# Optimization experiments

Measured on AMD Instinct MI355X. Metric: run time of the kernel, lower is better.

The kernel has to match this reference:

```python
import jax, jax.numpy as jnp
import numpy as np
from jax import lax

WIN_SIZE = 11
SIGMA = 1.5
WEIGHTS = jnp.array([0.0448, 0.2856, 0.3001, 0.2363, 0.1333], dtype=jnp.float32)
C1 = (0.01 * 1.0) ** 2  # val_range = 1.0
C2 = (0.03 * 1.0) ** 2


def gaussian_kernel2d(kernel_size, sigma):
    g = jnp.arange(kernel_size, dtype=jnp.float32) - kernel_size // 2
    g = jnp.exp(-(g ** 2) / (2.0 * sigma ** 2))
    g = g / g.sum()
    return jnp.outer(g, g)  # [k, k]


def depthwise_conv(x, k2d):
    # x: [B, C, H, W]; same gaussian window applied per-channel (groups=C), VALID padding
    C = x.shape[1]
    w = jnp.broadcast_to(k2d, (C, 1) + k2d.shape).astype(x.dtype)
    return lax.conv_general_dilated(x, w, (1, 1), 'VALID',
                                    feature_group_count=C,
                                    dimension_numbers=('NCHW', 'OIHW', 'NCHW'))


def ssim_index(x, y, k2d, nonnegative=True):
    # returns (ss, cs) each of shape [B, C] (spatial mean, per channel)
    m1 = depthwise_conv(x, k2d)
    m2 = depthwise_conv(y, k2d)
    m12 = m1 * m2
    m1s = m1 * m1
    m2s = m2 * m2
    v1 = depthwise_conv(x * x, k2d) - m1s
    v2 = depthwise_conv(y * y, k2d) - m2s
    cov = depthwise_conv(x * y, k2d) - m12
    cs = (2.0 * cov + C2) / (v1 + v2 + C2)
    ss = (2.0 * m12 + C1) / (m1s + m2s + C1) * cs
    ss = ss.reshape(ss.shape[0], ss.shape[1], -1).mean(axis=-1)
    cs = cs.reshape(cs.shape[0], cs.shape[1], -1).mean(axis=-1)
    if nonnegative:
        ss = jnp.maximum(ss, 0.0)
        cs = jnp.maximum(cs, 0.0)
    return ss, cs


def avg_pool2(x):
    # F.avg_pool2d(kernel_size=2). Input spatial dims are even at every scale
    # (512 -> 32), so ceil_mode never pads; plain 2x2/2 mean pooling is exact.
    s = lax.reduce_window(x, jnp.array(0.0, x.dtype), lax.add,
                          (1, 1, 2, 2), (1, 1, 2, 2), 'VALID')
    return s * 0.25


def setup_inputs() -> dict:
    key = jax.random.key(0)
    k1, k2 = jax.random.split(key)
    B, C, H, W = 4, 12, 512, 512
    pred = jax.random.normal(k1, (B, C, H, W), dtype=jnp.float32)
    target = jax.random.randint(k2, (B, H, W), 0, C, dtype=jnp.int64)
    return {"pred": pred, "target": target}


def reference(pred, target):
    # MS_SSIMLoss.forward with process_input=True, nonnegative=True.
    # The per-class python loop in the original is an independent depthwise
    # computation per channel -> vectorized here as a C-channel grouped conv;
    # loss = mean over classes of (1 - mean over batch of msss) == 1 - mean(msss).
    num_classes = pred.shape[1]
    x = jax.nn.softmax(pred, axis=1)
    y = jax.nn.one_hot(target, num_classes, dtype=pred.dtype).transpose(0, 3, 1, 2)
    k2d = gaussian_kernel2d(WIN_SIZE, SIGMA)
    m = WEIGHTS.shape[0]
    vals = []
    for i in range(m):
        if i > 0:
            x = avg_pool2(x)
            y = avg_pool2(y)
        ss, cs = ssim_index(x, y, k2d, nonnegative=True)
        vals.append(cs if i + 1 < m else ss)
    stacked = jnp.stack(vals, axis=-1)  # [B, C, m]
    msss = jnp.prod(stacked ** WEIGHTS, axis=-1)  # [B, C]
    return 1.0 - msss.mean()
```

## Files before the change

kernel.cpp:

```cpp
#include <hip/hip_runtime.h>

#define NCH 12
#define NB  4
#define BC  48
#define HW0 (512 * 512)

#define GK_INIT { 0.00102840f, 0.00759863f, 0.03600078f, 0.10936081f, \
                  0.21300541f, 0.26601164f, 0.21300541f, 0.10936081f, \
                  0.03600078f, 0.00759863f, 0.00102840f }

__global__ __launch_bounds__(256)
void k_prep(const float* __restrict__ pred, const int* __restrict__ tgt,
            float* __restrict__ U, float* __restrict__ X1,
            unsigned short* __restrict__ Y1, double* __restrict__ acc) {
    if (blockIdx.x == 0) {
        for (int t = threadIdx.x; t < 480; t += 256) acc[t] = 0.0;
    }
    const int blk = blockIdx.x;
    const int b  = blk >> 8;
    const int py = blk & 255;
    const int px = threadIdx.x;
    const size_t o00 = (size_t)(2 * py) * 512 + 2 * px;
    const size_t o10 = o00 + 512;
    const float* Pb = pred + (size_t)b * NCH * HW0;

    float s00 = 0.f, s01 = 0.f, s10 = 0.f, s11 = 0.f;
#pragma unroll
    for (int c = 0; c < NCH; ++c) {
        const float* pc = Pb + (size_t)c * HW0;
        float2 r0 = *(const float2*)(pc + o00);
        float2 r1 = *(const float2*)(pc + o10);
        s00 += __expf(r0.x); s01 += __expf(r0.y);
        s10 += __expf(r1.x); s11 += __expf(r1.y);
    }
    float u00 = 1.f / s00, u01 = 1.f / s01, u10 = 1.f / s10, u11 = 1.f / s11;
    float* Ub = U + (size_t)b * HW0;
    *(float2*)(Ub + o00) = make_float2(u00, u01);
    *(float2*)(Ub + o10) = make_float2(u10, u11);

    const int* Tb = tgt + (size_t)b * HW0;
    int2 t0 = *(const int2*)(Tb + o00);
    int2 t1 = *(const int2*)(Tb + o10);

#pragma unroll
    for (int c = 0; c < NCH; ++c) {
        const float* pc = Pb + (size_t)c * HW0;
        float2 r0 = *(const float2*)(pc + o00);
        float2 r1 = *(const float2*)(pc + o10);
        float xs = __expf(r0.x) * u00 + __expf(r0.y) * u01
                 + __expf(r1.x) * u10 + __expf(r1.y) * u11;
        size_t oidx = ((size_t)(b * NCH + c) * 256 + py) * 256 + px;
        X1[oidx] = 0.25f * xs;
        unsigned cnt = (unsigned)(t0.x == c) + (unsigned)(t0.y == c)
                     + (unsigned)(t1.x == c) + (unsigned)(t1.y == c);
        Y1[oidx] = (unsigned short)(cnt << 6);
    }
}

union SMem {
    struct {
        float sx[42 * 43 + 4];
        uint2 tm4[42 * 35];
        unsigned long long ybits[30];
        float red[8];
    } s0;
    struct {
        float sx[42 * 43 + 4];
        uint2 tm4[42 * 35];
        unsigned short tm5[42 * 35];
        unsigned short syu[42 * 43 + 4];
        float red[8];
    } rg;
};

__device__ __forceinline__ void ssim0_tile(
    const float* __restrict__ pred, const float* __restrict__ U,
    const int* __restrict__ tgt, double* __restrict__ acc,
    int tile, int bc,
    float* sx, uint2* tm4, unsigned long long* ybits, float* red) {
    constexpr int SS = 43;
    constexpr int TS = 35;
    constexpr int H = 512, W = 512, OH = 502, OW = 502, tilesX = 16;
    const float gk[11] = GK_INIT;

    const int ty = tile / tilesX, tx = tile - ty * tilesX;
    const int oy = ty * 32, ox = tx * 32;
    const int tid = threadIdx.x;
    const bool interior = (oy + 41 < H) && (ox + 41 < W);

    const int b = bc / NCH, cls = bc - (bc / NCH) * NCH;
    const float* Pb = pred + (((size_t)b * NCH + cls) << 18);
    const float* Ub = U + ((size_t)b << 18);
    const int* Tb = tgt + ((size_t)b << 18);

    {
        int r = tid / 42, c = tid - (tid / 42) * 42;
#pragma unroll
        for (int k = 0; k < 7; ++k) {
            bool inr = (k < 6) || (tid < 228);
            int gy = oy + r, gx = ox + c;
            bool ld = inr && (interior || (gy < H && gx < W));
            float xv = 0.f;
            bool bit = false;
            if (ld) {
                int off = gy * W + gx;
                xv = expf(Pb[off]) * Ub[off];
                bit = (Tb[off] == cls);
            }
            unsigned long long mk = __ballot(bit);
            if ((tid & 63) == 0) ybits[(tid >> 6) + (k << 2)] = mk;
            if (inr) sx[r * SS + c] = xv;
            c += 4; r += 6;
            if (c >= 42) { c -= 42; r += 1; }
        }
        if (tid == 0) { ybits[28] = 0ull; ybits[29] = 0ull; }
    }
    __syncthreads();

    if (tid < 252) {
        int rr = tid / 6, s = tid - (tid / 6) * 6;
        int c0 = s * 6;
        const float* px = sx + rr * SS + c0;
        float ac0[6] = {}, ac1[6] = {}, ac2[6] = {}, ac3[6] = {};
        unsigned long long win;
        {
            int i0 = rr * 42 + c0;
            int w = i0 >> 6, sh = i0 & 63;
            unsigned long long lo = ybits[w], hi = ybits[w + 1];
            win = sh ? ((lo >> sh) | (hi << (64 - sh))) : lo;
        }
#pragma unroll
        for (int j = 0; j < 16; ++j) {
            float xv = px[j];
            float xx = xv * xv;
            bool bit = (win >> j) & 1;
            float yv = bit ? 1.f : 0.f;
            float xy = bit ? xv : 0.f;
#pragma unroll
            for (int o = 0; o < 6; ++o) {
                int kk = j - o;
                if (kk >= 0 && kk <= 10) {
                    float g = gk[kk];
                    ac0[o] = fmaf(g, xv, ac0[o]);
                    ac1[o] = fmaf(g, yv, ac1[o]);
                    ac2[o] = fmaf(g, xx, ac2[o]);
                    ac3[o] = fmaf(g, xy, ac3[o]);
                }
            }
        }
        int ob = rr * TS + c0;
#pragma unroll
        for (int o = 0; o < 6; ++o) {
            if (c0 + o < 32) {
                unsigned ua = __float_as_uint(ac0[o]);
                unsigned ub = __float_as_uint(ac1[o]);
                unsigned uc = __float_as_uint(ac2[o]);
                unsigned ud = __float_as_uint(ac3[o]);
                tm4[ob + o] = make_uint2((ua >> 16) | (ub & 0xFFFF0000u),
                                         (uc >> 16) | (ud & 0xFFFF0000u));
            }
        }
    }
    __syncthreads();

    const float C1 = 1e-4f, C2 = 9e-4f;
    const int cc = tid & 31, rg = tid >> 5, r0 = rg << 2;
    float a0[4] = {}, a1[4] = {}, a2[4] = {}, a3[4] = {};
    const int vb = r0 * TS + cc;
#pragma unroll
    for (int k = 0; k < 14; ++k) {
        uint2 tv = tm4[vb + k * TS];
        float m1v = __uint_as_float(tv.x << 16);
        float m2v = __uint_as_float(tv.x & 0xFFFF0000u);
        float xxv = __uint_as_float(tv.y << 16);
        float xyv = __uint_as_float(tv.y & 0xFFFF0000u);
#pragma unroll
        for (int j = 0; j < 4; ++j) {
            int kk = k - j;
            if (kk >= 0 && kk <= 10) {
                float g = gk[kk];
                a0[j] = fmaf(g, m1v, a0[j]);
                a1[j] = fmaf(g, m2v, a1[j]);
                a2[j] = fmaf(g, xxv, a2[j]);
                a3[j] = fmaf(g, xyv, a3[j]);
            }
        }
    }
    float cs_l = 0.f, ss_l = 0.f;
    const bool colok = (ox + cc < OW);
#pragma unroll
    for (int j = 0; j < 4; ++j) {
        if (colok && (oy + r0 + j < OH)) {
            float m1 = a0[j], m2 = a1[j];
            float sxx = a2[j], sxy_ = a3[j];
            float m11 = m1 * m1, m22 = m2 * m2, m12 = m1 * m2;
            float v1 = sxx - m11, v2 = m2 - m22, cov = sxy_ - m12;
            float d1 = m11 + m22 + C1, d2 = v1 + v2 + C2;
            float n2 = 2.f * cov + C2;
            float q = 1.f / (d1 * d2);
            cs_l = fmaf(n2 * d1, q, cs_l);
            ss_l = fmaf((2.f * m12 + C1) * n2, q, ss_l);
        }
    }

    for (int off = 32; off; off >>= 1) {
        cs_l += __shfl_down(cs_l, off);
        ss_l += __shfl_down(ss_l, off);
    }
    int wv = tid >> 6, ln = tid & 63;
    if (ln == 0) { red[wv] = cs_l; red[4 + wv] = ss_l; }
    __syncthreads();
    if (tid == 0) {
        double cs_b = (double)red[0] + (double)red[1] + (double)red[2] + (double)red[3];
        double ss_b = (double)red[4] + (double)red[5] + (double)red[6] + (double)red[7];
        atomicAdd(&acc[bc], cs_b);
        atomicAdd(&acc[48 + bc], ss_b);
    }
}

template <int PIN>
__device__ __forceinline__ void ssim_tile_g(
    const float* __restrict__ Xs, const unsigned short* __restrict__ Ys,
    int H, int W, int OH, int OW, int tilesX, int tile, int bc,
    double* __restrict__ acc, int scale,
    float* sx, uint2* tm4, unsigned short* tm5, unsigned short* syu, float* red) {
    constexpr int SS = 43;
    constexpr int TS = 35;
    const float gk[11] = GK_INIT;

    const int ty = tile / tilesX, tx = tile - ty * tilesX;
    const int oy = ty * 32, ox = tx * 32;
    const int tid = threadIdx.x;
    const bool interior = (oy + 41 < H) && (ox + 41 < W);

    constexpr int SC = 1 << PIN;
    const int SW = W * SC;
    const float* Xb = Xs + (size_t)bc * H * W * SC * SC;
    const unsigned short* Yb = Ys + (size_t)bc * H * W * SC * SC;

    {
        int r = tid / 42, c = tid - (tid / 42) * 42;
#pragma unroll
        for (int k = 0; k < 7; ++k) {
            bool inr = (k < 6) || (tid < 228);
            int gy = oy + r, gx = ox + c;
            bool ld = inr && (interior || (gy < H && gx < W));
            float xv = 0.f;
            unsigned short yv = 0;
            if (ld) {
                if constexpr (PIN == 0) {
                    int off = gy * SW + gx;
                    xv = Xb[off];
                    yv = Yb[off];
                } else {
                    const float* q = Xb + (SC * gy) * SW + SC * gx;
                    const unsigned short* qy = Yb + (SC * gy) * SW + SC * gx;
                    float s = 0.f; unsigned us = 0;
#pragma unroll
                    for (int a = 0; a < SC; ++a) {
                        const float* qr = q + a * SW;
                        const unsigned short* qyr = qy + a * SW;
                        if constexpr (PIN == 1) {
                            float2 f = *(const float2*)qr;
                            s += f.x + f.y;
                            ushort2 uy = *(const ushort2*)qyr;
                            us += (unsigned)uy.x + (unsigned)uy.y;
                        } else {
#pragma unroll
                            for (int e4 = 0; e4 < SC / 4; ++e4) {
                                float4 f = *(const float4*)(qr + e4 * 4);
                                s += (f.x + f.y) + (f.z + f.w);
                                ushort4 uy = *(const ushort4*)(qyr + e4 * 4);
                                us += ((unsigned)uy.x + (unsigned)uy.y)
                                    + ((unsigned)uy.z + (unsigned)uy.w);
                            }
                        }
                    }
                    xv = s * (1.f / (float)(SC * SC));
                    yv = (unsigned short)(us >> (2 * PIN));
                }
            }
            if (inr) { sx[r * SS + c] = xv; syu[r * SS + c] = yv; }
            c += 4; r += 6;
            if (c >= 42) { c -= 42; r += 1; }
        }
    }
    __syncthreads();

    if (tid < 252) {
        int rr = tid / 6, s = tid - (tid / 6) * 6;
        int c0 = s * 6;
        const float* px = sx + rr * SS + c0;
        const unsigned short* pyu = syu + rr * SS + c0;
        float ac0[6] = {}, ac1[6] = {}, ac2[6] = {}, ac3[6] = {}, ac4[6] = {};
#pragma unroll
        for (int j = 0; j < 16; ++j) {
            float xv = px[j];
            float xx = xv * xv;
            float yv = (float)pyu[j];
            float xy = xv * yv;
            float yy = yv * yv;
#pragma unroll
            for (int o = 0; o < 6; ++o) {
                int kk = j - o;
                if (kk >= 0 && kk <= 10) {
                    float g = gk[kk];
                    ac0[o] = fmaf(g, xv, ac0[o]);
                    ac1[o] = fmaf(g, yv, ac1[o]);
                    ac2[o] = fmaf(g, xx, ac2[o]);
                    ac3[o] = fmaf(g, xy, ac3[o]);
                    ac4[o] = fmaf(g, yy, ac4[o]);
                }
            }
        }
        int ob = rr * TS + c0;
#pragma unroll
        for (int o = 0; o < 6; ++o) {
            if (c0 + o < 32) {
                unsigned ua = __float_as_uint(ac0[o]) + 0x8000u;
                unsigned ub = __float_as_uint(ac1[o]) + 0x8000u;
                unsigned uc = __float_as_uint(ac2[o]) + 0x8000u;
                unsigned ud = __float_as_uint(ac3[o]) + 0x8000u;
                unsigned ue = __float_as_uint(ac4[o]) + 0x8000u;
                tm4[ob + o] = make_uint2((ua >> 16) | (ub & 0xFFFF0000u),
                                         (uc >> 16) | (ud & 0xFFFF0000u));
                tm5[ob + o] = (unsigned short)(ue >> 16);
            }
        }
    }
    __syncthreads();

    const float C1 = 1e-4f, C2 = 9e-4f;
    const int cc = tid & 31, rg = tid >> 5, r0 = rg << 2;
    float a0[4] = {}, a1[4] = {}, a2[4] = {}, a3[4] = {}, a4[4] = {};
    const int vb = r0 * TS + cc;
#pragma unroll
    for (int k = 0; k < 14; ++k) {
        uint2 tv = tm4[vb + k * TS];
        float t0 = __uint_as_float(tv.x << 16);
        float t1 = __uint_as_float(tv.x & 0xFFFF0000u);
        float t2 = __uint_as_float(tv.y << 16);
        float t3 = __uint_as_float(tv.y & 0xFFFF0000u);
        float t4 = __uint_as_float((unsigned)tm5[vb + k * TS] << 16);
#pragma unroll
        for (int j = 0; j < 4; ++j) {
            int kk = k - j;
            if (kk >= 0 && kk <= 10) {
                float g = gk[kk];
                a0[j] = fmaf(g, t0, a0[j]);
                a1[j] = fmaf(g, t1, a1[j]);
                a2[j] = fmaf(g, t2, a2[j]);
                a3[j] = fmaf(g, t3, a3[j]);
                a4[j] = fmaf(g, t4, a4[j]);
            }
        }
    }
    float cs_l = 0.f, ss_l = 0.f;
    const bool colok = (ox + cc < OW);
#pragma unroll
    for (int j = 0; j < 4; ++j) {
        if (colok && (oy + r0 + j < OH)) {
            float m1 = a0[j];
            float m2 = a1[j] * (1.f / 256.f);
            float sxx = a2[j];
            float sxy_ = a3[j] * (1.f / 256.f);
            float syy_ = a4[j] * (1.f / 65536.f);
            float m11 = m1 * m1, m22 = m2 * m2, m12 = m1 * m2;
            float v1 = sxx - m11, v2 = syy_ - m22, cov = sxy_ - m12;
            float d1 = m11 + m22 + C1, d2 = v1 + v2 + C2;
            float n2 = 2.f * cov + C2;
            float q = 1.f / (d1 * d2);
            cs_l = fmaf(n2 * d1, q, cs_l);
            ss_l = fmaf((2.f * m12 + C1) * n2, q, ss_l);
        }
    }

    for (int offs = 32; offs; offs >>= 1) {
        cs_l += __shfl_down(cs_l, offs);
        ss_l += __shfl_down(ss_l, offs);
    }
    int wv = tid >> 6, ln = tid & 63;
    if (ln == 0) { red[wv] = cs_l; red[4 + wv] = ss_l; }
    __syncthreads();
    if (tid == 0) {
        double cs_b = (double)red[0] + (double)red[1] + (double)red[2] + (double)red[3];
        double ss_b = (double)red[4] + (double)red[5] + (double)red[6] + (double)red[7];
        atomicAdd(&acc[scale * 96 + bc], cs_b);
        atomicAdd(&acc[scale * 96 + 48 + bc], ss_b);
    }
}

__global__ __launch_bounds__(256, 6)
void k_main(const float* __restrict__ pred, const float* __restrict__ U,
            const int* __restrict__ tgt,
            const float* __restrict__ X1, const unsigned short* __restrict__ Y1,
            double* __restrict__ acc) {
    __shared__ SMem sm;
    const int gb = blockIdx.x;

    int s0_idx = -1, rest_idx = -1;
    if (gb < 16320) {
        int r = gb & 3, q = gb >> 2;
        if (r == 0) rest_idx = q;
        else        s0_idx = 3 * q + (r - 1);
    } else {
        s0_idx = 12240 + (gb - 16320);
    }

    if (s0_idx >= 0) {
        ssim0_tile(pred, U, tgt, acc, s0_idx & 255, s0_idx >> 8,
                   sm.s0.sx, sm.s0.tm4, sm.s0.ybits, sm.s0.red);
        return;
    }
    const int gq = rest_idx;
    if (gq < 48) {
        ssim_tile_g<3>(X1, Y1, 32, 32, 22, 22, 1, 0, gq,
                       acc, 4, sm.rg.sx, sm.rg.tm4, sm.rg.tm5, sm.rg.syu, sm.rg.red);
    } else if (gq < 240) {
        int t = gq - 48;
        ssim_tile_g<2>(X1, Y1, 64, 64, 54, 54, 2, t & 3, t >> 2,
                       acc, 3, sm.rg.sx, sm.rg.tm4, sm.rg.tm5, sm.rg.syu, sm.rg.red);
    } else if (gq < 1008) {
        int t = gq - 240;
        ssim_tile_g<1>(X1, Y1, 128, 128, 118, 118, 4, t & 15, t >> 4,
                       acc, 2, sm.rg.sx, sm.rg.tm4, sm.rg.tm5, sm.rg.syu, sm.rg.red);
    } else {
        int t = gq - 1008;
        ssim_tile_g<0>(X1, Y1, 256, 256, 246, 246, 8, t & 63, t >> 6,
                       acc, 1, sm.rg.sx, sm.rg.tm4, sm.rg.tm5, sm.rg.syu, sm.rg.red);
    }
}

__global__ void k_final(const double* __restrict__ acc, float* __restrict__ out) {
    const float wts[5] = {0.0448f, 0.2856f, 0.3001f, 0.2363f, 0.1333f};
    const float cnt[5] = {252004.f, 60516.f, 13924.f, 2916.f, 484.f};
    int tid = threadIdx.x;
    float msss = 0.f;
    if (tid < BC) {
        msss = 1.f;
#pragma unroll
        for (int s = 0; s < 5; ++s) {
            double a = (s < 4) ? acc[s * 96 + tid] : acc[s * 96 + 48 + tid];
            float v = fmaxf((float)(a / (double)cnt[s]), 0.f);
            msss *= powf(v, wts[s]);
        }
    }
    for (int off = 32; off; off >>= 1) msss += __shfl_down(msss, off);
    if (tid == 0) out[0] = 1.f - msss * (1.f / (float)BC);
}

extern "C" void kernel_launch(void* const* d_in, const int* in_sizes, int n_in,
                              void* d_out, int out_size, void* d_ws, size_t ws_size,
                              hipStream_t stream) {
    const float* pred = (const float*)d_in[0];
    const int*   tgt  = (const int*)d_in[1];
    float* out = (float*)d_out;

    double* acc = (double*)d_ws;
    float* U  = (float*)(acc + 480);
    float* X1 = U + (size_t)NB * HW0;
    unsigned short* Y1 = (unsigned short*)(X1 + (size_t)BC * 65536);

    k_prep<<<1024, 256, 0, stream>>>(pred, tgt, U, X1, Y1, acc);

    k_main<<<16368, 256, 0, stream>>>(pred, U, tgt, X1, Y1, acc);

    k_final<<<1, 64, 0, stream>>>(acc, out);
}
```

Before: 235.4 us.

## Cache softmax exps, pack x/y into one LDS word, fast exp, raise occupancy

k_prep now keeps the 12 per-channel exponentials in registers instead of reloading pred and recomputing exp in a second pass. In the coarse-scale tiles, x is rounded to bf16 and packed with the y count into a single 32-bit LDS word, which shrinks shared memory and halves LDS reads in the conv loop. Scale 0 switches expf to __expf, and launch bounds go from 6 to 7 blocks per CU. The bf16 rounding of x and the fast exp lower accuracy, and the tighter register cap could cause spills.

```diff
diff --git a/kernel.cpp b/kernel.cpp
--- a/kernel.cpp
+++ b/kernel.cpp
@@ -24,14 +24,16 @@
     const size_t o10 = o00 + 512;
     const float* Pb = pred + (size_t)b * NCH * HW0;
 
+    float ex[NCH], ey[NCH], ez[NCH], ew[NCH];
     float s00 = 0.f, s01 = 0.f, s10 = 0.f, s11 = 0.f;
 #pragma unroll
     for (int c = 0; c < NCH; ++c) {
         const float* pc = Pb + (size_t)c * HW0;
         float2 r0 = *(const float2*)(pc + o00);
         float2 r1 = *(const float2*)(pc + o10);
-        s00 += __expf(r0.x); s01 += __expf(r0.y);
-        s10 += __expf(r1.x); s11 += __expf(r1.y);
+        ex[c] = __expf(r0.x); ey[c] = __expf(r0.y);
+        ez[c] = __expf(r1.x); ew[c] = __expf(r1.y);
+        s00 += ex[c]; s01 += ey[c]; s10 += ez[c]; s11 += ew[c];
     }
     float u00 = 1.f / s00, u01 = 1.f / s01, u10 = 1.f / s10, u11 = 1.f / s11;
     float* Ub = U + (size_t)b * HW0;
@@ -44,11 +46,7 @@
 
 #pragma unroll
     for (int c = 0; c < NCH; ++c) {
-        const float* pc = Pb + (size_t)c * HW0;
-        float2 r0 = *(const float2*)(pc + o00);
-        float2 r1 = *(const float2*)(pc + o10);
-        float xs = __expf(r0.x) * u00 + __expf(r0.y) * u01
-                 + __expf(r1.x) * u10 + __expf(r1.y) * u11;
+        float xs = ex[c] * u00 + ey[c] * u01 + ez[c] * u10 + ew[c] * u11;
         size_t oidx = ((size_t)(b * NCH + c) * 256 + py) * 256 + px;
         X1[oidx] = 0.25f * xs;
         unsigned cnt = (unsigned)(t0.x == c) + (unsigned)(t0.y == c)
@@ -65,10 +63,9 @@
         float red[8];
     } s0;
     struct {
-        float sx[42 * 43 + 4];
+        unsigned int sxy[42 * 43 + 4];
         uint2 tm4[42 * 35];
         unsigned short tm5[42 * 35];
-        unsigned short syu[42 * 43 + 4];
         float red[8];
     } rg;
 };
@@ -104,7 +101,7 @@
             bool bit = false;
             if (ld) {
                 int off = gy * W + gx;
-                xv = expf(Pb[off]) * Ub[off];
+                xv = __expf(Pb[off]) * Ub[off];
                 bit = (Tb[off] == cls);
             }
             unsigned long long mk = __ballot(bit);
@@ -223,7 +220,7 @@
     const float* __restrict__ Xs, const unsigned short* __restrict__ Ys,
     int H, int W, int OH, int OW, int tilesX, int tile, int bc,
     double* __restrict__ acc, int scale,
-    float* sx, uint2* tm4, unsigned short* tm5, unsigned short* syu, float* red) {
+    unsigned int* sxy, uint2* tm4, unsigned short* tm5, float* red) {
     constexpr int SS = 43;
     constexpr int TS = 35;
     const float gk[11] = GK_INIT;
@@ -246,12 +243,12 @@
             int gy = oy + r, gx = ox + c;
             bool ld = inr && (interior || (gy < H && gx < W));
             float xv = 0.f;
-            unsigned short yv = 0;
+            unsigned yc = 0;
             if (ld) {
                 if constexpr (PIN == 0) {
                     int off = gy * SW + gx;
                     xv = Xb[off];
-                    yv = Yb[off];
+                    yc = Yb[off];
                 } else {
                     const float* q = Xb + (SC * gy) * SW + SC * gx;
                     const unsigned short* qy = Yb + (SC * gy) * SW + SC * gx;
@@ -277,10 +274,13 @@
                         }
                     }
                     xv = s * (1.f / (float)(SC * SC));
-                    yv = (unsigned short)(us >> (2 * PIN));
+                    yc = us >> (2 * PIN);
                 }
             }
-            if (inr) { sx[r * SS + c] = xv; syu[r * SS + c] = yv; }
+            if (inr) {
+                unsigned xb = (__float_as_uint(xv) + 0x8000u) >> 16;
+                sxy[r * SS + c] = (yc << 16) | xb;
+            }
             c += 4; r += 6;
             if (c >= 42) { c -= 42; r += 1; }
         }
@@ -290,14 +290,14 @@
     if (tid < 252) {
         int rr = tid / 6, s = tid - (tid / 6) * 6;
         int c0 = s * 6;
-        const float* px = sx + rr * SS + c0;
-        const unsigned short* pyu = syu + rr * SS + c0;
+        const unsigned int* pxy = sxy + rr * SS + c0;
         float ac0[6] = {}, ac1[6] = {}, ac2[6] = {}, ac3[6] = {}, ac4[6] = {};
 #pragma unroll
         for (int j = 0; j < 16; ++j) {
-            float xv = px[j];
+            unsigned v = pxy[j];
+            float xv = __uint_as_float(v << 16);
+            float yv = (float)(v >> 16);
             float xx = xv * xv;
-            float yv = (float)pyu[j];
             float xy = xv * yv;
             float yy = yv * yv;
 #pragma unroll
@@ -390,7 +390,7 @@
     }
 }
 
-__global__ __launch_bounds__(256, 6)
+__global__ __launch_bounds__(256, 7)
 void k_main(const float* __restrict__ pred, const float* __restrict__ U,
             const int* __restrict__ tgt,
             const float* __restrict__ X1, const unsigned short* __restrict__ Y1,
@@ -415,19 +415,19 @@
     const int gq = rest_idx;
     if (gq < 48) {
         ssim_tile_g<3>(X1, Y1, 32, 32, 22, 22, 1, 0, gq,
-                       acc, 4, sm.rg.sx, sm.rg.tm4, sm.rg.tm5, sm.rg.syu, sm.rg.red);
+                       acc, 4, sm.rg.sxy, sm.rg.tm4, sm.rg.tm5, sm.rg.red);
     } else if (gq < 240) {
         int t = gq - 48;
         ssim_tile_g<2>(X1, Y1, 64, 64, 54, 54, 2, t & 3, t >> 2,
-                       acc, 3, sm.rg.sx, sm.rg.tm4, sm.rg.tm5, sm.rg.syu, sm.rg.red);
+                       acc, 3, sm.rg.sxy, sm.rg.tm4, sm.rg.tm5, sm.rg.red);
     } else if (gq < 1008) {
         int t = gq - 240;
         ssim_tile_g<1>(X1, Y1, 128, 128, 118, 118, 4, t & 15, t >> 4,
-                       acc, 2, sm.rg.sx, sm.rg.tm4, sm.rg.tm5, sm.rg.syu, sm.rg.red);
+                       acc, 2, sm.rg.sxy, sm.rg.tm4, sm.rg.tm5, sm.rg.red);
     } else {
         int t = gq - 1008;
         ssim_tile_g<0>(X1, Y1, 256, 256, 246, 246, 8, t & 63, t >> 6,
-                       acc, 1, sm.rg.sx, sm.rg.tm4, sm.rg.tm5, sm.rg.syu, sm.rg.red);
+                       acc, 1, sm.rg.sxy, sm.rg.tm4, sm.rg.tm5, sm.rg.red);
     }
 }
 
```

Result: faster. 222.3 us (-5.6%).
